# Kernel optimization log

Measured on AMD Instinct MI355X. Metric: run time of the kernel, lower is better.

Reference implementation:

```python
import jax, jax.numpy as jnp
import numpy as np

N = 50000
E = 800000


def gcn_conv(x, W, b, src, dst, norm):
    # x: [N, Fin] -> [N, Fout]; PyG GCNConv: linear, normalized scatter-add, bias
    h = x @ W                                  # [N, Fout]
    msg = h[src] * norm[:, None]               # [E+N, Fout] gather + scale
    out = jax.ops.segment_sum(msg, dst, num_segments=N)  # scatter-add
    return out + b


def _with_self_loops(edge_index):
    loops = jnp.arange(N, dtype=edge_index.dtype)
    src = jnp.concatenate([edge_index[0], loops])
    dst = jnp.concatenate([edge_index[1], loops])
    return src, dst


def _gcn_norm(src, dst):
    deg = jax.ops.segment_sum(jnp.ones_like(src, dtype=jnp.float32), dst, num_segments=N)
    dinv = jnp.where(deg > 0, jax.lax.rsqrt(jnp.maximum(deg, 1.0)), 0.0)
    return dinv[src] * dinv[dst]


def setup_inputs() -> dict:
    key = jax.random.key(0)
    ks = jax.random.split(key, 8)
    x = jax.random.normal(ks[0], (N, 128), dtype=jnp.float32)
    edge_index = jax.random.randint(ks[1], (2, E), 0, N, dtype=jnp.int64)
    # Glorot-ish init for the three GCNConv layers
    W1 = jax.random.normal(ks[2], (128, 64), dtype=jnp.float32) * (1.0 / np.sqrt(128))
    b1 = jnp.zeros((64,), dtype=jnp.float32)
    W2 = jax.random.normal(ks[3], (64, 64), dtype=jnp.float32) * (1.0 / np.sqrt(64))
    b2 = jnp.zeros((64,), dtype=jnp.float32)
    W3 = jax.random.normal(ks[4], (64, 40), dtype=jnp.float32) * (1.0 / np.sqrt(64))
    b3 = jnp.zeros((40,), dtype=jnp.float32)
    return {"x": x, "edge_index": edge_index, "W1": W1, "b1": b1,
            "W2": W2, "b2": b2, "W3": W3, "b3": b3}


def reference(x, edge_index, W1, b1, W2, b2, W3, b3):
    src, dst = _with_self_loops(edge_index)
    norm = _gcn_norm(src, dst)
    h = jax.nn.relu(gcn_conv(x, W1, b1, src, dst, norm))
    h = jax.nn.relu(gcn_conv(h, W2, b2, src, dst, norm))
    return gcn_conv(h, W3, b3, src, dst, norm)
```

## Files before the change

kernel.cpp:

```cpp
#include <hip/hip_runtime.h>

#define NNODE 50000
#define NEDGE 800000
#define NBUCKET 196
#define NPB 256
#define EPB 3125

typedef __attribute__((ext_vector_type(8))) unsigned short ushort8v;

__device__ inline unsigned short f2bf(float f) {
    unsigned int u = __float_as_uint(f);
    u += 0x7FFFu + ((u >> 16) & 1u);
    return (unsigned short)(u >> 16);
}
__device__ inline float bf2f(unsigned short h) {
    return __uint_as_float((unsigned int)h << 16);
}


__global__ __launch_bounds__(256) void k_histA(const int* __restrict__ dst, int* __restrict__ hist_g) {
    __shared__ int h[NBUCKET];
    const int tid = threadIdx.x, pb = blockIdx.x, e0 = pb * EPB;
    if (tid < NBUCKET) h[tid] = 0;
    __syncthreads();
    for (int i = tid; i < EPB; i += 256)
        atomicAdd(&h[dst[e0 + i] >> 8], 1);
    __syncthreads();
    if (tid < NBUCKET) hist_g[tid * 256 + pb] = h[tid];
}

__global__ __launch_bounds__(256) void k_scanA1(const int* __restrict__ hist_g, int* __restrict__ base_g,
                                                int* __restrict__ colsum) {
    __shared__ int s[256];
    const int b = blockIdx.x, t = threadIdx.x;
    int v = hist_g[b * 256 + t];
    s[t] = v;
    __syncthreads();
#pragma unroll
    for (int off = 1; off < 256; off <<= 1) {
        int a = (t >= off) ? s[t - off] : 0;
        __syncthreads();
        s[t] += a;
        __syncthreads();
    }
    base_g[b * 256 + t] = s[t] - v;
    if (t == 255) colsum[b] = s[t];
}

__global__ __launch_bounds__(256) void k_scanA2(const int* __restrict__ colsum, int* __restrict__ bucketbase,
                                                int* __restrict__ rowstart) {
    __shared__ int s[256];
    const int t = threadIdx.x;
    int v = (t < NBUCKET) ? colsum[t] : 0;
    s[t] = v;
    __syncthreads();
#pragma unroll
    for (int off = 1; off < 256; off <<= 1) {
        int a = (t >= off) ? s[t - off] : 0;
        __syncthreads();
        s[t] += a;
        __syncthreads();
    }
    if (t < NBUCKET) bucketbase[t] = s[t] - v;
    if (t == 0) { bucketbase[NBUCKET] = NEDGE; rowstart[NNODE] = NEDGE; }
}

__global__ __launch_bounds__(256) void k_scatterA(const int* __restrict__ src, const int* __restrict__ dst,
                          const int* __restrict__ base_g, const int* __restrict__ bucketbase,
                          unsigned int* __restrict__ bucketed) {
    __shared__ int cur[NBUCKET];
    const int tid = threadIdx.x, pb = blockIdx.x, e0 = pb * EPB;
    if (tid < NBUCKET) cur[tid] = bucketbase[tid] + base_g[tid * 256 + pb];
    __syncthreads();
    for (int i = tid; i < EPB; i += 256) {
        int d = dst[e0 + i], s = src[e0 + i];
        int pos = atomicAdd(&cur[d >> 8], 1);
        bucketed[pos] = ((unsigned int)d << 16) | (unsigned int)s;
    }
}


__global__ __launch_bounds__(256) void k_bucketB2(const unsigned int* __restrict__ bucketed,
                          const int* __restrict__ bucketbase, int* __restrict__ rowstart,
                          int* __restrict__ csr_src, float* __restrict__ dinv) {
    __shared__ int cnt[NPB];
    __shared__ int ex[NPB];
    __shared__ int cur[NPB];
    const int tid = threadIdx.x, b = blockIdx.x;
    const int base_out = bucketbase[b], end_out = bucketbase[b + 1];

    cnt[tid] = 0;
    __syncthreads();
    for (int i = base_out + tid; i < end_out; i += 256)
        atomicAdd(&cnt[(bucketed[i] >> 16) & 255], 1);
    __syncthreads();

    int v = cnt[tid];
    ex[tid] = v;
    __syncthreads();
#pragma unroll
    for (int off = 1; off < 256; off <<= 1) {
        int a = (tid >= off) ? ex[tid - off] : 0;
        __syncthreads();
        ex[tid] += a;
        __syncthreads();
    }
    int excl = ex[tid] - v;
    int node = (b << 8) + tid;
    cur[tid] = base_out + excl;
    if (node < NNODE) {
        rowstart[node] = base_out + excl;
        dinv[node] = rsqrtf((float)v + 1.0f);
    }
    __syncthreads();

    for (int i = base_out + tid; i < end_out; i += 256) {
        unsigned int u = bucketed[i];
        int pos = atomicAdd(&cur[(u >> 16) & 255], 1);
        csr_src[pos] = (int)(u & 0xFFFFu);
    }
}


template<int FIN, int FOUT>
__launch_bounds__(256)
__global__ void k_gemm_prescale(const float* __restrict__ X, const float* __restrict__ W,
                                const float* __restrict__ dinv, unsigned short* __restrict__ XWs) {
    __shared__ float Xt[FIN * 68];
    __shared__ float Ws[FIN * 64];

    const int tid = threadIdx.x;
    const int r0 = blockIdx.x * 64;

    for (int idx = tid; idx < FIN * 64; idx += 256) {
        int k = idx >> 6, c = idx & 63;
        Ws[idx] = (c < FOUT) ? W[k * FOUT + c] : 0.0f;
    }

    constexpr int CH = FIN / 4;
    constexpr int CSH = (FIN == 128) ? 5 : 4;
    for (int idx = tid; idx < 64 * CH; idx += 256) {
        int r_lo = idx & 7;
        int c = (idx >> 3) & (CH - 1);
        int r = ((idx >> (3 + CSH)) << 3) + r_lo;
        int rr = r0 + r; if (rr >= NNODE) rr = NNODE - 1;
        float4 v = *(const float4*)(X + (size_t)rr * FIN + c * 4);
        Xt[(4 * c + 0) * 68 + r] = v.x;
        Xt[(4 * c + 1) * 68 + r] = v.y;
        Xt[(4 * c + 2) * 68 + r] = v.z;
        Xt[(4 * c + 3) * 68 + r] = v.w;
    }
    __syncthreads();

    const int cg = tid & 15;
    const int rg = tid >> 4;

    float acc[4][4] = {};
#pragma unroll 4
    for (int k = 0; k < FIN; ++k) {
        float4 xv = *(const float4*)&Xt[k * 68 + 4 * rg];
        float4 wv = *(const float4*)&Ws[k * 64 + 4 * cg];
#pragma unroll
        for (int i = 0; i < 4; ++i) {
            float xi = (i == 0) ? xv.x : (i == 1) ? xv.y : (i == 2) ? xv.z : xv.w;
            acc[i][0] = fmaf(xi, wv.x, acc[i][0]);
            acc[i][1] = fmaf(xi, wv.y, acc[i][1]);
            acc[i][2] = fmaf(xi, wv.z, acc[i][2]);
            acc[i][3] = fmaf(xi, wv.w, acc[i][3]);
        }
    }

    if (4 * cg + 4 <= FOUT) {
#pragma unroll
        for (int i = 0; i < 4; ++i) {
            int row = r0 + 4 * rg + i;
            if (row < NNODE) {
                float dv = dinv[row];
                ushort4 o = { f2bf(acc[i][0] * dv), f2bf(acc[i][1] * dv),
                              f2bf(acc[i][2] * dv), f2bf(acc[i][3] * dv) };
                *(ushort4*)(XWs + (size_t)row * FOUT + 4 * cg) = o;
            }
        }
    }
}


template<int F, bool RELU>
__launch_bounds__(256)
__global__ void k_aggregate(const unsigned short* __restrict__ XWs, const int* __restrict__ rowstart,
                            const int* __restrict__ csr_src, const float* __restrict__ dinv,
                            const float* __restrict__ b, float* __restrict__ out) {
    constexpr int NQ = F / 8;
    const int wid  = threadIdx.x >> 6;
    const int lane = threadIdx.x & 63;
    const int g = lane >> 3;
    const int q = lane & 7;
    const int d = blockIdx.x * 4 + wid;
    if (d >= NNODE) return;

    const int beg = rowstart[d];
    const int end = rowstart[d + 1];
    const bool qa = (q < NQ);

    float acc[8] = {};

    for (int base = beg; base < end; base += 64) {
        int idx = base + lane;
        int sv = (idx < end) ? csr_src[idx] : 0;
        int nv = min(64, end - base);
        for (int j = 0; j < nv; j += 8) {
            int jj = j + g;
            int s = __shfl(sv, jj);
            if (jj < nv && qa) {
                ushort8v v = *(const ushort8v*)(XWs + (size_t)s * F + 8 * q);
#pragma unroll
                for (int t = 0; t < 8; ++t) acc[t] += bf2f(v[t]);
            }
        }
    }

#pragma unroll
    for (int mask = 8; mask <= 32; mask <<= 1) {
#pragma unroll
        for (int t = 0; t < 8; ++t) acc[t] += __shfl_xor(acc[t], mask);
    }

    if (g == 0 && qa) {
        ushort8v self = *(const ushort8v*)(XWs + (size_t)d * F + 8 * q);
        float dv = dinv[d];
        float o[8];
#pragma unroll
        for (int t = 0; t < 8; ++t) {
            o[t] = fmaf(acc[t] + bf2f(self[t]), dv, b[8 * q + t]);
            if (RELU) o[t] = fmaxf(o[t], 0.f);
        }
        float4 o0 = { o[0], o[1], o[2], o[3] };
        float4 o1 = { o[4], o[5], o[6], o[7] };
        *(float4*)(out + (size_t)d * F + 8 * q)     = o0;
        *(float4*)(out + (size_t)d * F + 8 * q + 4) = o1;
    }
}

extern "C" void kernel_launch(void* const* d_in, const int* in_sizes, int n_in,
                              void* d_out, int out_size, void* d_ws, size_t ws_size,
                              hipStream_t stream) {
    const float* x  = (const float*)d_in[0];
    const int*   ei = (const int*)d_in[1];
    const float* W1 = (const float*)d_in[2];
    const float* b1 = (const float*)d_in[3];
    const float* W2 = (const float*)d_in[4];
    const float* b2 = (const float*)d_in[5];
    const float* W3 = (const float*)d_in[6];
    const float* b3 = (const float*)d_in[7];
    float* out = (float*)d_out;

    const int* src = ei;
    const int* dst = ei + NEDGE;

    char* p = (char*)d_ws;
    auto alloc = [&](size_t bytes) { char* r = p; p += (bytes + 255) & ~size_t(255); return r; };
    unsigned int* bucketed = (unsigned int*)alloc((size_t)NEDGE * 4);
    int*   hist_g     = (int*)  alloc(NBUCKET * 256 * 4);
    int*   base_g     = (int*)  alloc(NBUCKET * 256 * 4);
    int*   colsum     = (int*)  alloc(NBUCKET * 4);
    int*   bucketbase = (int*)  alloc((NBUCKET + 1) * 4);
    int*   rowstart   = (int*)  alloc((NNODE + 1) * 4);
    int*   csr_src    = (int*)  alloc((size_t)NEDGE * 4);
    float* dinv       = (float*)alloc(NNODE * 4);
    unsigned short* XWs = (unsigned short*)alloc((size_t)NNODE * 64 * 2 + 256);
    float* H1         = (float*)alloc((size_t)NNODE * 64 * 4);
    float* H2         = (float*)alloc((size_t)NNODE * 64 * 4);

    const int B = 256;
    const int gGemm = (NNODE + 63) / 64;
    const int gAgg  = (NNODE + 3) / 4;

    k_histA   <<<256, B, 0, stream>>>(dst, hist_g);
    k_scanA1  <<<NBUCKET, B, 0, stream>>>(hist_g, base_g, colsum);
    k_scanA2  <<<1, B, 0, stream>>>(colsum, bucketbase, rowstart);
    k_scatterA<<<256, B, 0, stream>>>(src, dst, base_g, bucketbase, bucketed);
    k_bucketB2<<<NBUCKET, B, 0, stream>>>(bucketed, bucketbase, rowstart, csr_src, dinv);

    k_gemm_prescale<128, 64><<<gGemm, B, 0, stream>>>(x, W1, dinv, XWs);
    k_aggregate<64, true><<<gAgg, B, 0, stream>>>(XWs, rowstart, csr_src, dinv, b1, H1);

    k_gemm_prescale<64, 64><<<gGemm, B, 0, stream>>>(H1, W2, dinv, XWs);
    k_aggregate<64, true><<<gAgg, B, 0, stream>>>(XWs, rowstart, csr_src, dinv, b2, H2);

    k_gemm_prescale<64, 40><<<gGemm, B, 0, stream>>>(H2, W3, dinv, XWs);
    k_aggregate<40, false><<<gAgg, B, 0, stream>>>(XWs, rowstart, csr_src, dinv, b3, out);
}
```

Before: 159.8 us.

## Fold bucket scan into consumers, store CSR as ushort and hidden layers as bf16

Removes the single-block scan kernel by having the scatter and bucket kernels each redo the 196-entry column-sum scan in shared memory. The CSR source index array shrinks to 16-bit, which relies on node ids fitting in 16 bits. With N=50000 that already holds in the packed bucket word. Intermediate activations H1/H2 are now written and read as bf16 instead of fp32, cutting gather and GEMM input traffic at the cost of extra rounding.

Measured after the change: 158.1 us. Within noise of the previous version (-1.1%).

```diff
diff --git a/kernel.cpp b/kernel.cpp
--- a/kernel.cpp
+++ b/kernel.cpp
@@ -47,30 +47,29 @@
     if (t == 255) colsum[b] = s[t];
 }
 
-__global__ __launch_bounds__(256) void k_scanA2(const int* __restrict__ colsum, int* __restrict__ bucketbase,
-                                                int* __restrict__ rowstart) {
-    __shared__ int s[256];
-    const int t = threadIdx.x;
-    int v = (t < NBUCKET) ? colsum[t] : 0;
-    s[t] = v;
+__device__ inline void scan_colsum(const int* __restrict__ colsum, int* cs, int tid) {
+    cs[tid] = (tid < NBUCKET) ? colsum[tid] : 0;
     __syncthreads();
 #pragma unroll
     for (int off = 1; off < 256; off <<= 1) {
-        int a = (t >= off) ? s[t - off] : 0;
-        __syncthreads();
-        s[t] += a;
-        __syncthreads();
-    }
-    if (t < NBUCKET) bucketbase[t] = s[t] - v;
-    if (t == 0) { bucketbase[NBUCKET] = NEDGE; rowstart[NNODE] = NEDGE; }
+        int a = (tid >= off) ? cs[tid - off] : 0;
+        __syncthreads();
+        cs[tid] += a;
+        __syncthreads();
+    }
 }
 
 __global__ __launch_bounds__(256) void k_scatterA(const int* __restrict__ src, const int* __restrict__ dst,
-                          const int* __restrict__ base_g, const int* __restrict__ bucketbase,
+                          const int* __restrict__ base_g, const int* __restrict__ colsum,
                           unsigned int* __restrict__ bucketed) {
+    __shared__ int cs[256];
     __shared__ int cur[NBUCKET];
     const int tid = threadIdx.x, pb = blockIdx.x, e0 = pb * EPB;
-    if (tid < NBUCKET) cur[tid] = bucketbase[tid] + base_g[tid * 256 + pb];
+    scan_colsum(colsum, cs, tid);
+    if (tid < NBUCKET) {
+        int bb = (tid == 0) ? 0 : cs[tid - 1];
+        cur[tid] = bb + base_g[tid * 256 + pb];
+    }
     __syncthreads();
     for (int i = tid; i < EPB; i += 256) {
         int d = dst[e0 + i], s = src[e0 + i];
@@ -81,13 +80,16 @@
 
 
 __global__ __launch_bounds__(256) void k_bucketB2(const unsigned int* __restrict__ bucketed,
-                          const int* __restrict__ bucketbase, int* __restrict__ rowstart,
-                          int* __restrict__ csr_src, float* __restrict__ dinv) {
+                          const int* __restrict__ colsum, int* __restrict__ rowstart,
+                          unsigned short* __restrict__ csr_src, float* __restrict__ dinv) {
+    __shared__ int cs[256];
     __shared__ int cnt[NPB];
     __shared__ int ex[NPB];
     __shared__ int cur[NPB];
     const int tid = threadIdx.x, b = blockIdx.x;
-    const int base_out = bucketbase[b], end_out = bucketbase[b + 1];
+    scan_colsum(colsum, cs, tid);
+    const int base_out = (b == 0) ? 0 : cs[b - 1];
+    const int end_out  = cs[b];
 
     cnt[tid] = 0;
     __syncthreads();
@@ -112,19 +114,20 @@
         rowstart[node] = base_out + excl;
         dinv[node] = rsqrtf((float)v + 1.0f);
     }
+    if (b == 0 && tid == 0) rowstart[NNODE] = NEDGE;
     __syncthreads();
 
     for (int i = base_out + tid; i < end_out; i += 256) {
         unsigned int u = bucketed[i];
         int pos = atomicAdd(&cur[(u >> 16) & 255], 1);
-        csr_src[pos] = (int)(u & 0xFFFFu);
-    }
-}
-
-
-template<int FIN, int FOUT>
+        csr_src[pos] = (unsigned short)(u & 0xFFFFu);
+    }
+}
+
+
+template<int FIN, int FOUT, typename XT>
 __launch_bounds__(256)
-__global__ void k_gemm_prescale(const float* __restrict__ X, const float* __restrict__ W,
+__global__ void k_gemm_prescale(const XT* __restrict__ X, const float* __restrict__ W,
                                 const float* __restrict__ dinv, unsigned short* __restrict__ XWs) {
     __shared__ float Xt[FIN * 68];
     __shared__ float Ws[FIN * 64];
@@ -137,18 +140,33 @@
         Ws[idx] = (c < FOUT) ? W[k * FOUT + c] : 0.0f;
     }
 
-    constexpr int CH = FIN / 4;
-    constexpr int CSH = (FIN == 128) ? 5 : 4;
-    for (int idx = tid; idx < 64 * CH; idx += 256) {
-        int r_lo = idx & 7;
-        int c = (idx >> 3) & (CH - 1);
-        int r = ((idx >> (3 + CSH)) << 3) + r_lo;
-        int rr = r0 + r; if (rr >= NNODE) rr = NNODE - 1;
-        float4 v = *(const float4*)(X + (size_t)rr * FIN + c * 4);
-        Xt[(4 * c + 0) * 68 + r] = v.x;
-        Xt[(4 * c + 1) * 68 + r] = v.y;
-        Xt[(4 * c + 2) * 68 + r] = v.z;
-        Xt[(4 * c + 3) * 68 + r] = v.w;
+    if constexpr (sizeof(XT) == 4) {
+        constexpr int CH = FIN / 4;
+        constexpr int CSH = (FIN == 128) ? 5 : 4;
+        for (int idx = tid; idx < 64 * CH; idx += 256) {
+            int r_lo = idx & 7;
+            int c = (idx >> 3) & (CH - 1);
+            int r = ((idx >> (3 + CSH)) << 3) + r_lo;
+            int rr = r0 + r; if (rr >= NNODE) rr = NNODE - 1;
+            float4 v = *(const float4*)((const float*)X + (size_t)rr * FIN + c * 4);
+            Xt[(4 * c + 0) * 68 + r] = v.x;
+            Xt[(4 * c + 1) * 68 + r] = v.y;
+            Xt[(4 * c + 2) * 68 + r] = v.z;
+            Xt[(4 * c + 3) * 68 + r] = v.w;
+        }
+    } else {
+        constexpr int CH = FIN / 8;
+        constexpr int CSH = (FIN == 128) ? 4 : 3;
+        for (int idx = tid; idx < 64 * CH; idx += 256) {
+            int r_lo = idx & 7;
+            int c = (idx >> 3) & (CH - 1);
+            int r = ((idx >> (3 + CSH)) << 3) + r_lo;
+            int rr = r0 + r; if (rr >= NNODE) rr = NNODE - 1;
+            ushort8v v = *(const ushort8v*)((const unsigned short*)X + (size_t)rr * FIN + c * 8);
+#pragma unroll
+            for (int t = 0; t < 8; ++t)
+                Xt[(8 * c + t) * 68 + r] = bf2f(v[t]);
+        }
     }
     __syncthreads();
 
@@ -185,11 +203,11 @@
 }
 
 
-template<int F, bool RELU>
+template<int F, bool RELU, bool OUTBF>
 __launch_bounds__(256)
 __global__ void k_aggregate(const unsigned short* __restrict__ XWs, const int* __restrict__ rowstart,
-                            const int* __restrict__ csr_src, const float* __restrict__ dinv,
-                            const float* __restrict__ b, float* __restrict__ out) {
+                            const unsigned short* __restrict__ csr_src, const float* __restrict__ dinv,
+                            const float* __restrict__ b, void* __restrict__ outp) {
     constexpr int NQ = F / 8;
     const int wid  = threadIdx.x >> 6;
     const int lane = threadIdx.x & 63;
@@ -206,7 +224,7 @@
 
     for (int base = beg; base < end; base += 64) {
         int idx = base + lane;
-        int sv = (idx < end) ? csr_src[idx] : 0;
+        int sv = (idx < end) ? (int)csr_src[idx] : 0;
         int nv = min(64, end - base);
         for (int j = 0; j < nv; j += 8) {
             int jj = j + g;
@@ -234,10 +252,17 @@
             o[t] = fmaf(acc[t] + bf2f(self[t]), dv, b[8 * q + t]);
             if (RELU) o[t] = fmaxf(o[t], 0.f);
         }
-        float4 o0 = { o[0], o[1], o[2], o[3] };
-        float4 o1 = { o[4], o[5], o[6], o[7] };
-        *(float4*)(out + (size_t)d * F + 8 * q)     = o0;
-        *(float4*)(out + (size_t)d * F + 8 * q + 4) = o1;
+        if (OUTBF) {
+            ushort8v ov;
+#pragma unroll
+            for (int t = 0; t < 8; ++t) ov[t] = f2bf(o[t]);
+            *(ushort8v*)((unsigned short*)outp + (size_t)d * F + 8 * q) = ov;
+        } else {
+            float4 o0 = { o[0], o[1], o[2], o[3] };
+            float4 o1 = { o[4], o[5], o[6], o[7] };
+            *(float4*)((float*)outp + (size_t)d * F + 8 * q)     = o0;
+            *(float4*)((float*)outp + (size_t)d * F + 8 * q + 4) = o1;
+        }
     }
 }
 
@@ -263,13 +288,12 @@
     int*   hist_g     = (int*)  alloc(NBUCKET * 256 * 4);
     int*   base_g     = (int*)  alloc(NBUCKET * 256 * 4);
     int*   colsum     = (int*)  alloc(NBUCKET * 4);
-    int*   bucketbase = (int*)  alloc((NBUCKET + 1) * 4);
     int*   rowstart   = (int*)  alloc((NNODE + 1) * 4);
-    int*   csr_src    = (int*)  alloc((size_t)NEDGE * 4);
+    unsigned short* csr_src = (unsigned short*)alloc((size_t)NEDGE * 2);
     float* dinv       = (float*)alloc(NNODE * 4);
     unsigned short* XWs = (unsigned short*)alloc((size_t)NNODE * 64 * 2 + 256);
-    float* H1         = (float*)alloc((size_t)NNODE * 64 * 4);
-    float* H2         = (float*)alloc((size_t)NNODE * 64 * 4);
+    unsigned short* H1  = (unsigned short*)alloc((size_t)NNODE * 64 * 2 + 256);
+    unsigned short* H2  = (unsigned short*)alloc((size_t)NNODE * 64 * 2 + 256);
 
     const int B = 256;
     const int gGemm = (NNODE + 63) / 64;
@@ -277,16 +301,15 @@
 
     k_histA   <<<256, B, 0, stream>>>(dst, hist_g);
     k_scanA1  <<<NBUCKET, B, 0, stream>>>(hist_g, base_g, colsum);
-    k_scanA2  <<<1, B, 0, stream>>>(colsum, bucketbase, rowstart);
-    k_scatterA<<<256, B, 0, stream>>>(src, dst, base_g, bucketbase, bucketed);
-    k_bucketB2<<<NBUCKET, B, 0, stream>>>(bucketed, bucketbase, rowstart, csr_src, dinv);
-
-    k_gemm_prescale<128, 64><<<gGemm, B, 0, stream>>>(x, W1, dinv, XWs);
-    k_aggregate<64, true><<<gAgg, B, 0, stream>>>(XWs, rowstart, csr_src, dinv, b1, H1);
-
-    k_gemm_prescale<64, 64><<<gGemm, B, 0, stream>>>(H1, W2, dinv, XWs);
-    k_aggregate<64, true><<<gAgg, B, 0, stream>>>(XWs, rowstart, csr_src, dinv, b2, H2);
-
-    k_gemm_prescale<64, 40><<<gGemm, B, 0, stream>>>(H2, W3, dinv, XWs);
-    k_aggregate<40, false><<<gAgg, B, 0, stream>>>(XWs, rowstart, csr_src, dinv, b3, out);
-}
+    k_scatterA<<<256, B, 0, stream>>>(src, dst, base_g, colsum, bucketed);
+    k_bucketB2<<<NBUCKET, B, 0, stream>>>(bucketed, colsum, rowstart, csr_src, dinv);
+
+    k_gemm_prescale<128, 64, float><<<gGemm, B, 0, stream>>>(x, W1, dinv, XWs);
+    k_aggregate<64, true, true><<<gAgg, B, 0, stream>>>(XWs, rowstart, csr_src, dinv, b1, H1);
+
+    k_gemm_prescale<64, 64, unsigned short><<<gGemm, B, 0, stream>>>(H1, W2, dinv, XWs);
+    k_aggregate<64, true, true><<<gAgg, B, 0, stream>>>(XWs, rowstart, csr_src, dinv, b2, H2);
+
+    k_gemm_prescale<64, 40, unsigned short><<<gGemm, B, 0, stream>>>(H2, W3, dinv, XWs);
+    k_aggregate<40, false, false><<<gAgg, B, 0, stream>>>(XWs, rowstart, csr_src, dinv, b3, out);
+}
```
